# Kernel tuning notes

Hardware: AMD Instinct MI355X
Metric: run time of the kernel (lower is better)

The kernel has to match this reference:

```python
import jax, jax.numpy as jnp
import numpy as np

NUM_EXPERTS = 64
TOP_K = 2
AUX_COEF = 0.01
Z_COEF = 0.001
INIT_STD = 0.02


def setup_inputs() -> dict:
    key = jax.random.key(0)
    k1, k2 = jax.random.split(key)
    B, S, D = 4, 4096, 2048
    x = jax.random.normal(k1, (B, S, D), dtype=jnp.float32)
    gate_w = jax.random.normal(k2, (NUM_EXPERTS, D), dtype=jnp.float32) * INIT_STD
    return {"x": x, "gate_w": gate_w}


def reference(x, gate_w):
    B, S, D = x.shape
    E, K = NUM_EXPERTS, TOP_K
    # gate linear: (B,S,D) @ (D,E) -> (B,S,E), cast to fp32 like .float()
    logits = jnp.einsum('bsd,ed->bse', x, gate_w).astype(jnp.float32)
    weights = jax.nn.softmax(logits, axis=-1)
    top_weights, top_indices = jax.lax.top_k(weights, K)
    top_weights = top_weights / jnp.sum(top_weights, axis=-1, keepdims=True)
    # load-balance aux loss (training branch)
    flat_idx = top_indices.reshape(-1)
    tokens_per_expert = jax.ops.segment_sum(
        jnp.ones_like(flat_idx, dtype=jnp.float32), flat_idx, num_segments=E)
    f = tokens_per_expert / (B * S * K)
    P = jnp.mean(weights, axis=(0, 1))
    balance_loss = E * jnp.sum(f * P)
    z_loss = jnp.mean(jnp.square(jax.nn.logsumexp(logits, axis=-1)))
    aux_loss = AUX_COEF * balance_loss + Z_COEF * z_loss
    return top_indices, top_weights, aux_loss
```

## Files before the change

### kernel.cpp

```cpp
#include <hip/hip_runtime.h>
#include <math.h>

#define NTOK 16384
#define DDIM 2048
#define NEXP 64
#define NKQ 16
#define KSLICE 128
#define TPB 64

typedef __attribute__((ext_vector_type(8))) short bf16x8;
typedef __attribute__((ext_vector_type(4))) float f32x4;


__device__ __forceinline__ void split3pk(float a, float b,
                                         unsigned &H, unsigned &M, unsigned &L) {
    asm("v_cvt_pk_bf16_f32 %0, %1, %2" : "=v"(H) : "v"(a), "v"(b));
    float ra = a - __builtin_bit_cast(float, H << 16);
    float rb = b - __builtin_bit_cast(float, H & 0xffff0000u);
    asm("v_cvt_pk_bf16_f32 %0, %1, %2" : "=v"(M) : "v"(ra), "v"(rb));
    float sa = ra - __builtin_bit_cast(float, M << 16);
    float sb = rb - __builtin_bit_cast(float, M & 0xffff0000u);
    asm("v_cvt_pk_bf16_f32 %0, %1, %2" : "=v"(L) : "v"(sa), "v"(sb));
}

__device__ __forceinline__ void keepf(float4 &v) {
    asm volatile("" : "+v"(v.x), "+v"(v.y), "+v"(v.z), "+v"(v.w));
}

__global__ void k_wpack(const float* __restrict__ gw, unsigned short* __restrict__ wp) {
    int idx = blockIdx.x * 256 + threadIdx.x;
    int lane = idx & 63;
    int ks   = (idx >> 6) & 63;
    int eg   = idx >> 12;
    int e  = eg * 16 + (lane & 15);
    int k0 = ks * 32 + (lane >> 4) * 8;
    const float* src = gw + (size_t)e * DDIM + k0;
    uint4 H, M, L;
    split3pk(src[0], src[1], H.x, M.x, L.x);
    split3pk(src[2], src[3], H.y, M.y, L.y);
    split3pk(src[4], src[5], H.z, M.z, L.z);
    split3pk(src[6], src[7], H.w, M.w, L.w);
    size_t fb = ((size_t)ks * 12 + eg * 3) * 512 + lane * 8;
    *(uint4*)(wp + fb)        = H;
    *(uint4*)(wp + fb + 512)  = M;
    *(uint4*)(wp + fb + 1024) = L;
}

__global__ __launch_bounds__(256, 2)
void k_gemm(const float* __restrict__ x, const unsigned short* __restrict__ wp,
            float* __restrict__ part) {
    __shared__ __align__(16) char Ws[49152];

    const int tid  = threadIdx.x;
    const int kq   = blockIdx.x & 15;
    const int tok0 = (blockIdx.x >> 4) * TPB;
    const int lane = tid & 63;
    const int wvu  = __builtin_amdgcn_readfirstlane(tid >> 6);
    const int tau  = lane & 15;
    const int kap  = lane >> 4;

    {
        const char* wsrc = (const char*)wp + (size_t)kq * 49152;
        #pragma unroll
        for (int r = 0; r < 12; ++r) {
            const char* g = wsrc + (size_t)(r * 256 + tid) * 16;
            char* l = Ws + (size_t)(r * 256 + wvu * 64) * 16;
            __builtin_amdgcn_global_load_lds(
                (const __attribute__((address_space(1))) void*)g,
                (__attribute__((address_space(3))) void*)l, 16, 0, 0);
        }
    }

    const float* xb = x + (size_t)(tok0 + wvu * 16 + tau) * DDIM
                        + kq * KSLICE + kap * 8;
    float4 x0a = *(const float4*)(xb);
    float4 x0b = *(const float4*)(xb + 4);
    float4 x1a = *(const float4*)(xb + 32);
    float4 x1b = *(const float4*)(xb + 36);
    float4 x2a = *(const float4*)(xb + 64);
    float4 x2b = *(const float4*)(xb + 68);
    float4 x3a = *(const float4*)(xb + 96);
    float4 x3b = *(const float4*)(xb + 100);
    keepf(x0a); keepf(x0b); keepf(x1a); keepf(x1b);
    keepf(x2a); keepf(x2b); keepf(x3a); keepf(x3b);

    __syncthreads();

    f32x4 acc[4];
    #pragma unroll
    for (int eg = 0; eg < 4; ++eg) acc[eg] = (f32x4){0.f, 0.f, 0.f, 0.f};

    #pragma unroll
    for (int ks = 0; ks < 4; ++ks) {
        float4 a = (ks == 0) ? x0a : (ks == 1) ? x1a : (ks == 2) ? x2a : x3a;
        float4 b = (ks == 0) ? x0b : (ks == 1) ? x1b : (ks == 2) ? x2b : x3b;
        uint4 Ah, Am, Al;
        split3pk(a.x, a.y, Ah.x, Am.x, Al.x);
        split3pk(a.z, a.w, Ah.y, Am.y, Al.y);
        split3pk(b.x, b.y, Ah.z, Am.z, Al.z);
        split3pk(b.z, b.w, Ah.w, Am.w, Al.w);
        bf16x8 Ahv = __builtin_bit_cast(bf16x8, Ah);
        bf16x8 Amv = __builtin_bit_cast(bf16x8, Am);
        bf16x8 Alv = __builtin_bit_cast(bf16x8, Al);

        #pragma unroll
        for (int eg = 0; eg < 4; ++eg) {
            const char* wb = Ws + ks * 12288 + eg * 3072 + lane * 16;
            bf16x8 Bh = *(const bf16x8*)(wb);
            bf16x8 Bm = *(const bf16x8*)(wb + 1024);
            bf16x8 Bl = *(const bf16x8*)(wb + 2048);
            acc[eg] = __builtin_amdgcn_mfma_f32_16x16x32_bf16(Ahv, Bh, acc[eg], 0, 0, 0);
            acc[eg] = __builtin_amdgcn_mfma_f32_16x16x32_bf16(Ahv, Bm, acc[eg], 0, 0, 0);
            acc[eg] = __builtin_amdgcn_mfma_f32_16x16x32_bf16(Amv, Bh, acc[eg], 0, 0, 0);
            acc[eg] = __builtin_amdgcn_mfma_f32_16x16x32_bf16(Ahv, Bl, acc[eg], 0, 0, 0);
            acc[eg] = __builtin_amdgcn_mfma_f32_16x16x32_bf16(Alv, Bh, acc[eg], 0, 0, 0);
            acc[eg] = __builtin_amdgcn_mfma_f32_16x16x32_bf16(Amv, Bm, acc[eg], 0, 0, 0);
        }
    }

    float* pb = part + ((size_t)kq * NTOK + tok0 + wvu * 16) * 64;
    #pragma unroll
    for (int eg = 0; eg < 4; ++eg)
        #pragma unroll
        for (int j = 0; j < 4; ++j)
            pb[(kap * 4 + j) * 64 + eg * 16 + tau] = acc[eg][j];
}

__global__ __launch_bounds__(256, 2)
void k_reduce(const float* __restrict__ part, float* __restrict__ out,
              float* __restrict__ gcnt, float* __restrict__ gP,
              float* __restrict__ gz) {
    __shared__ float Ps[NEXP], Cnt[NEXP], Zs;
    const int tid = threadIdx.x;
    if (tid < NEXP) { Ps[tid] = 0.f; Cnt[tid] = 0.f; }
    if (tid == 0) Zs = 0.f;
    __syncthreads();

    const int lane = tid & 63;
    const int wv   = tid >> 6;
    const int t0   = blockIdx.x * 16 + wv * 4;

    float l4[4] = {0.f, 0.f, 0.f, 0.f};
    #pragma unroll
    for (int q = 0; q < NKQ; ++q)
        #pragma unroll
        for (int i = 0; i < 4; ++i)
            l4[i] += part[((size_t)q * NTOK + t0 + i) * 64 + lane];

    float Pacc = 0.f, zacc = 0.f;
    #pragma unroll
    for (int i = 0; i < 4; ++i) {
        float l = l4[i];
        float mx = l;
        #pragma unroll
        for (int off = 32; off > 0; off >>= 1) mx = fmaxf(mx, __shfl_xor(mx, off));
        float s = expf(l - mx);
        float sum = s;
        #pragma unroll
        for (int off = 32; off > 0; off >>= 1) sum += __shfl_xor(sum, off);
        Pacc += s / sum;

        unsigned long long b1 = __ballot(l == mx);
        int i1 = __ffsll(b1) - 1;
        float l2 = (lane == i1) ? -INFINITY : l;
        float m2 = l2;
        #pragma unroll
        for (int off = 32; off > 0; off >>= 1) m2 = fmaxf(m2, __shfl_xor(m2, off));
        unsigned long long b2 = __ballot(l2 == m2);
        int i2 = __ffsll(b2) - 1;

        if (lane == 0) {
            float s2  = expf(m2 - mx);
            float inv = 1.f / (1.f + s2);
            int gt = t0 + i;
            ((float2*)out)[gt]              = make_float2((float)i1, (float)i2);
            ((float2*)(out + 2 * NTOK))[gt] = make_float2(inv, s2 * inv);
            atomicAdd(&Cnt[i1], 1.f);
            atomicAdd(&Cnt[i2], 1.f);
            float lse = mx + logf(sum);
            zacc += lse * lse;
        }
    }
    atomicAdd(&Ps[lane], Pacc);
    if (lane == 0) atomicAdd(&Zs, zacc);
    __syncthreads();

    if (tid < NEXP) {
        atomicAdd(&gcnt[tid], Cnt[tid]);
        atomicAdd(&gP[tid],   Ps[tid]);
    }
    if (tid == 0) atomicAdd(gz, Zs);
}

__global__ void k_final(const float* __restrict__ ws, float* __restrict__ out) {
    int lane = threadIdx.x;
    float v = ws[lane] * ws[64 + lane];
    #pragma unroll
    for (int off = 32; off > 0; off >>= 1) v += __shfl_xor(v, off);
    if (lane == 0) {
        float bal = 64.f * v / (32768.f * 16384.f);
        float z   = ws[128] / 16384.f;
        out[4 * NTOK] = 0.01f * bal + 0.001f * z;
    }
}

extern "C" void kernel_launch(void* const* d_in, const int* in_sizes, int n_in,
                              void* d_out, int out_size, void* d_ws, size_t ws_size,
                              hipStream_t stream) {
    const float* x  = (const float*)d_in[0];
    const float* gw = (const float*)d_in[1];
    float* out = (float*)d_out;
    float* wsf = (float*)d_ws;
    unsigned short* wp = (unsigned short*)((char*)d_ws + 1024);
    float* part = (float*)((char*)d_ws + (1 << 20));

    hipMemsetAsync(d_ws, 0, 516, stream);
    k_wpack<<<64, 256, 0, stream>>>(gw, wp);
    k_gemm<<<NKQ * (NTOK / TPB), 256, 0, stream>>>(x, wp, part);
    k_reduce<<<NTOK / 16, 256, 0, stream>>>(part, out, wsf, wsf + 64, wsf + 128);
    k_final<<<1, 64, 0, stream>>>(wsf, out);
}
```

Before: 83.63 us.

## Restructure reduce to 16 lanes per token with vector loads; fold memset into wpack

The reduce kernel now assigns 16 lanes to each token, with each lane owning 4 experts loaded as a float4. Top-2 selection is done with a 16-wide shuffle merge instead of repeated full-wave max reductions and ballots, which cuts shuffle and serial work per token. The memset of the aux accumulators is removed and done inside k_wpack, saving one launch. The trade-off is more LDS atomics on Ps (4 per lane) and a more involved tie-breaking merge.

```diff
diff --git a/kernel.cpp b/kernel.cpp
--- a/kernel.cpp
+++ b/kernel.cpp
@@ -27,7 +27,9 @@
     asm volatile("" : "+v"(v.x), "+v"(v.y), "+v"(v.z), "+v"(v.w));
 }
 
-__global__ void k_wpack(const float* __restrict__ gw, unsigned short* __restrict__ wp) {
+__global__ void k_wpack(const float* __restrict__ gw, unsigned short* __restrict__ wp,
+                        float* __restrict__ aux) {
+    if (blockIdx.x == 0 && threadIdx.x < 132) aux[threadIdx.x] = 0.f;
     int idx = blockIdx.x * 256 + threadIdx.x;
     int lane = idx & 63;
     int ks   = (idx >> 6) & 63;
@@ -138,51 +140,63 @@
 
     const int lane = tid & 63;
     const int wv   = tid >> 6;
-    const int t0   = blockIdx.x * 16 + wv * 4;
-
-    float l4[4] = {0.f, 0.f, 0.f, 0.f};
-    #pragma unroll
-    for (int q = 0; q < NKQ; ++q)
-        #pragma unroll
-        for (int i = 0; i < 4; ++i)
-            l4[i] += part[((size_t)q * NTOK + t0 + i) * 64 + lane];
-
-    float Pacc = 0.f, zacc = 0.f;
-    #pragma unroll
-    for (int i = 0; i < 4; ++i) {
-        float l = l4[i];
-        float mx = l;
-        #pragma unroll
-        for (int off = 32; off > 0; off >>= 1) mx = fmaxf(mx, __shfl_xor(mx, off));
-        float s = expf(l - mx);
-        float sum = s;
-        #pragma unroll
-        for (int off = 32; off > 0; off >>= 1) sum += __shfl_xor(sum, off);
-        Pacc += s / sum;
-
-        unsigned long long b1 = __ballot(l == mx);
-        int i1 = __ffsll(b1) - 1;
-        float l2 = (lane == i1) ? -INFINITY : l;
-        float m2 = l2;
-        #pragma unroll
-        for (int off = 32; off > 0; off >>= 1) m2 = fmaxf(m2, __shfl_xor(m2, off));
-        unsigned long long b2 = __ballot(l2 == m2);
-        int i2 = __ffsll(b2) - 1;
-
-        if (lane == 0) {
-            float s2  = expf(m2 - mx);
-            float inv = 1.f / (1.f + s2);
-            int gt = t0 + i;
-            ((float2*)out)[gt]              = make_float2((float)i1, (float)i2);
-            ((float2*)(out + 2 * NTOK))[gt] = make_float2(inv, s2 * inv);
-            atomicAdd(&Cnt[i1], 1.f);
-            atomicAdd(&Cnt[i2], 1.f);
-            float lse = mx + logf(sum);
-            zacc += lse * lse;
-        }
-    }
-    atomicAdd(&Ps[lane], Pacc);
-    if (lane == 0) atomicAdd(&Zs, zacc);
+    const int g    = lane >> 4;
+    const int s    = lane & 15;
+    const int t    = blockIdx.x * 16 + wv * 4 + g;
+    const int e4   = s * 4;
+
+    f32x4 a = {0.f, 0.f, 0.f, 0.f};
+    #pragma unroll
+    for (int q = 0; q < NKQ; ++q) {
+        const f32x4 v = *(const f32x4*)(part + ((size_t)q * NTOK + t) * 64 + e4);
+        a[0] += v[0]; a[1] += v[1]; a[2] += v[2]; a[3] += v[3];
+    }
+
+    float m1 = a[0], m2 = -INFINITY;
+    int   i1 = e4,   i2 = NEXP;
+    #pragma unroll
+    for (int j = 1; j < 4; ++j) {
+        float v = a[j]; int idx = e4 + j;
+        if (v > m1)      { m2 = m1; i2 = i1; m1 = v; i1 = idx; }
+        else if (v > m2) { m2 = v;  i2 = idx; }
+    }
+    #pragma unroll
+    for (int off = 1; off < 16; off <<= 1) {
+        float n1 = __shfl_xor(m1, off, 16);
+        int   j1 = __shfl_xor(i1, off, 16);
+        float n2 = __shfl_xor(m2, off, 16);
+        int   j2 = __shfl_xor(i2, off, 16);
+        bool pwin = (n1 > m1) || (n1 == m1 && j1 < i1);
+        float w1 = pwin ? n1 : m1;  int wi1 = pwin ? j1 : i1;
+        float c  = pwin ? m1 : n1;  int ci  = pwin ? i1 : j1;
+        float ws = pwin ? n2 : m2;  int wsi = pwin ? j2 : i2;
+        bool csec = (c > ws) || (c == ws && ci < wsi);
+        m1 = w1; i1 = wi1;
+        m2 = csec ? c : ws; i2 = csec ? ci : wsi;
+    }
+
+    float ex0 = expf(a[0] - m1), ex1 = expf(a[1] - m1);
+    float ex2 = expf(a[2] - m1), ex3 = expf(a[3] - m1);
+    float sum = (ex0 + ex1) + (ex2 + ex3);
+    #pragma unroll
+    for (int off = 1; off < 16; off <<= 1) sum += __shfl_xor(sum, off, 16);
+
+    float inv = 1.f / sum;
+    atomicAdd(&Ps[e4 + 0], ex0 * inv);
+    atomicAdd(&Ps[e4 + 1], ex1 * inv);
+    atomicAdd(&Ps[e4 + 2], ex2 * inv);
+    atomicAdd(&Ps[e4 + 3], ex3 * inv);
+
+    if (s == 0) {
+        float s2  = expf(m2 - m1);
+        float w1v = 1.f / (1.f + s2);
+        ((float2*)out)[t]              = make_float2((float)i1, (float)i2);
+        ((float2*)(out + 2 * NTOK))[t] = make_float2(w1v, s2 * w1v);
+        atomicAdd(&Cnt[i1], 1.f);
+        atomicAdd(&Cnt[i2], 1.f);
+        float lse = m1 + logf(sum);
+        atomicAdd(&Zs, lse * lse);
+    }
     __syncthreads();
 
     if (tid < NEXP) {
@@ -214,8 +228,7 @@
     unsigned short* wp = (unsigned short*)((char*)d_ws + 1024);
     float* part = (float*)((char*)d_ws + (1 << 20));
 
-    hipMemsetAsync(d_ws, 0, 516, stream);
-    k_wpack<<<64, 256, 0, stream>>>(gw, wp);
+    k_wpack<<<64, 256, 0, stream>>>(gw, wp, wsf);
     k_gemm<<<NKQ * (NTOK / TPB), 256, 0, stream>>>(x, wp, part);
     k_reduce<<<NTOK / 16, 256, 0, stream>>>(part, out, wsf, wsf + 64, wsf + 128);
     k_final<<<1, 64, 0, stream>>>(wsf, out);
```

After: 79.15 us. -5.4%, faster.
